# Kernel optimization log

Hardware: AMD Instinct MI355X
Metric: run time of the kernel (lower is better)

The kernel has to match this reference:

```python
import jax, jax.numpy as jnp
import numpy as np

DIM = 128      # link_state_dim
E = 100000     # num edges
P = 800000     # num adjacency pairs
G = 1000       # num graphs
T = 8          # message passing steps
R = 256        # readout_units


def setup_inputs() -> dict:
    key = jax.random.key(0)
    ks = jax.random.split(key, 16)
    s = lambda *shp: 1.0 / np.sqrt(shp[0])
    inp = {
        "link_state": jax.random.normal(ks[0], (E, DIM), dtype=jnp.float32),
        "states_graph_ids": jnp.sort(jax.random.randint(ks[1], (E,), 0, G, dtype=jnp.int32)),
        "states_first": jax.random.randint(ks[2], (P,), 0, E, dtype=jnp.int32),
        "states_second": jax.random.randint(ks[3], (P,), 0, E, dtype=jnp.int32),
        "sates_num_edges": E,
        # Message MLP: Dense(2*DIM -> DIM), selu
        "W_msg": jax.random.normal(ks[4], (2 * DIM, DIM), dtype=jnp.float32) * s(2 * DIM),
        "b_msg": jnp.zeros((DIM,), dtype=jnp.float32),
        # GRUCell (keras default reset_after=True): kernel/recurrent_kernel [DIM, 3*DIM], bias [2, 3*DIM]
        "gru_kernel": jax.random.normal(ks[5], (DIM, 3 * DIM), dtype=jnp.float32) * s(DIM),
        "gru_rec_kernel": jax.random.normal(ks[6], (DIM, 3 * DIM), dtype=jnp.float32) * s(DIM),
        "gru_bias": jnp.zeros((2, 3 * DIM), dtype=jnp.float32),
        # Readout MLP: DIM -> R -> R -> 1
        "W1": jax.random.normal(ks[7], (DIM, R), dtype=jnp.float32) * s(DIM),
        "b1": jnp.zeros((R,), dtype=jnp.float32),
        "W2": jax.random.normal(ks[8], (R, R), dtype=jnp.float32) * s(R),
        "b2": jnp.zeros((R,), dtype=jnp.float32),
        "W3": jax.random.normal(ks[9], (R, 1), dtype=jnp.float32) * s(R),
        "b3": jnp.zeros((1,), dtype=jnp.float32),
    }
    return inp


def _gru_cell(x, h, kernel, rec_kernel, bias):
    # Keras GRUCell, reset_after=True, gate order (z, r, h)
    mx = x @ kernel + bias[0]
    mh = h @ rec_kernel + bias[1]
    xz, xr, xh = jnp.split(mx, 3, axis=1)
    rz, rr, rh = jnp.split(mh, 3, axis=1)
    z = jax.nn.sigmoid(xz + rz)
    r = jax.nn.sigmoid(xr + rr)
    hh = jnp.tanh(xh + r * rh)
    return z * h + (1.0 - z) * hh


def reference(link_state, states_graph_ids, states_first, states_second, sates_num_edges,
              W_msg, b_msg, gru_kernel, gru_rec_kernel, gru_bias,
              W1, b1, W2, b2, W3, b3):
    for _ in range(T):
        # gather main & neighbor edge states, concat on feature dim -> [P, 2*DIM]
        edges_concat = jnp.concatenate([link_state[states_first], link_state[states_second]], axis=1)
        msgs = jax.nn.selu(edges_concat @ W_msg + b_msg)              # [P, DIM]
        agg = jax.ops.segment_sum(msgs, states_second, num_segments=sates_num_edges)  # [E, DIM]
        link_state = _gru_cell(agg, link_state, gru_kernel, gru_rec_kernel, gru_bias)
    pooled = jax.ops.segment_sum(link_state, states_graph_ids, num_segments=G)  # [G, DIM]
    h = jax.nn.selu(pooled @ W1 + b1)
    h = jax.nn.selu(h @ W2 + b2)
    return h @ W3 + b3  # [G, 1]
```

## Files before the change

### kernel.cpp

```cpp
#include <hip/hip_runtime.h>
#include <hip/hip_fp16.h>
#include <math.h>

#define DIM 128
#define E_NUM 100000
#define P_NUM 800000
#define G_NUM 1000
#define T_STEPS 8
#define R_UNITS 256

typedef __attribute__((ext_vector_type(8))) short bf16x8;
typedef __attribute__((ext_vector_type(4))) float f32x4;

typedef unsigned short ushort_t;
typedef unsigned int   uint_t;

__device__ __forceinline__ float selu_f(float x) {
    const float alpha = 1.6732632423543772f;
    const float scale = 1.0507009873554805f;
    return x > 0.f ? scale * x : scale * alpha * expm1f(x);
}

__device__ __forceinline__ float selu_fast(float x) {
    const float scale = 1.0507009873554805f;
    const float A     = 1.7580993408473766f;
    const float l2e   = 1.4426950408889634f;
    const float e = __builtin_amdgcn_exp2f(x * l2e);
    return x > 0.f ? scale * x : A * e - A;
}

__device__ __forceinline__ ushort_t f2bf(float x) {
    uint_t u = __float_as_uint(x);
    uint_t r = (u + 0x7fffu + ((u >> 16) & 1u)) >> 16;
    return (ushort_t)r;
}
__device__ __forceinline__ float bf2f(ushort_t h) {
    return __uint_as_float(((uint_t)h) << 16);
}

__global__ __launch_bounds__(256)
void hist_kernel(const int* __restrict__ second, int* __restrict__ counts)
{
    const int p = blockIdx.x * 256 + threadIdx.x;
    atomicAdd(&counts[second[p]], 1);
}

__global__ __launch_bounds__(1024)
void scanA_kernel(const int* __restrict__ counts, int* __restrict__ offsets,
                  int* __restrict__ bsum)
{
    __shared__ int buf[1024];
    const int i = blockIdx.x * 1024 + threadIdx.x;
    const int v = (i < E_NUM) ? counts[i] : 0;
    buf[threadIdx.x] = v;
    __syncthreads();
    for (int off = 1; off < 1024; off <<= 1) {
        const int t = (threadIdx.x >= off) ? buf[threadIdx.x - off] : 0;
        __syncthreads();
        buf[threadIdx.x] += t;
        __syncthreads();
    }
    if (i < E_NUM) offsets[i] = buf[threadIdx.x] - v;
    if (threadIdx.x == 1023) bsum[blockIdx.x] = buf[1023];
}

__global__ void scanB_kernel(int* __restrict__ bsum, int* __restrict__ offsets)
{
    int acc = 0;
    for (int b = 0; b < 98; b++) { const int t = bsum[b]; bsum[b] = acc; acc += t; }
    offsets[E_NUM] = P_NUM;
}

__global__ __launch_bounds__(1024)
void scanC_kernel(int* __restrict__ offsets, const int* __restrict__ bsum)
{
    const int i = blockIdx.x * 1024 + threadIdx.x;
    if (i < E_NUM) offsets[i] += bsum[blockIdx.x];
}

__global__ __launch_bounds__(256)
void fill_kernel(const int* __restrict__ first, const int* __restrict__ second,
                 const int* __restrict__ offsets, int* __restrict__ cursor,
                 int* __restrict__ sfirst, int* __restrict__ ssecond)
{
    const int p = blockIdx.x * 256 + threadIdx.x;
    const int d = second[p];
    const int pos = atomicAdd(&cursor[d], 1);
    const int idx = offsets[d] + pos;
    sfirst[idx] = first[p];
    ssecond[idx] = d;
}

__global__ __launch_bounds__(256)
void cast_h_kernel(const float* __restrict__ src,
                   ushort_t* __restrict__ dhi, ushort_t* __restrict__ dlo)
{
    const int idx = blockIdx.x * 256 + threadIdx.x;
    const float x = src[idx];
    const ushort_t hi = f2bf(x);
    dhi[idx] = hi;
    dlo[idx] = f2bf(x - bf2f(hi));
}

__global__ __launch_bounds__(256)
void wsplit_build_kernel(const float* __restrict__ Wmsg,
                         ushort_t* __restrict__ wt, ushort_t* __restrict__ wy)
{
    const int idx  = blockIdx.x * 256 + threadIdx.x;
    const int lane = idx & 63;
    const int nt   = (idx >> 6) & 7;
    const int comp = (idx >> 9) & 1;
    const int ks   = (idx >> 10) & 3;
    const int half = idx >> 12;
    const int n    = nt * 16 + (lane & 15);
    const int kb   = ks * 32 + (lane >> 4) * 8 + half * 128;
    ushort_t* dst  = half ? wy : wt;
    const int slot = idx & 4095;
#pragma unroll
    for (int j = 0; j < 8; j++) {
        const float w = Wmsg[(size_t)(kb + j) * DIM + n];
        const ushort_t hi = f2bf(w);
        dst[(size_t)slot * 8 + j] = comp ? f2bf(w - bf2f(hi)) : hi;
    }
}

__global__ __launch_bounds__(256)
void wb_build_kernel(const float* __restrict__ K, const float* __restrict__ U,
                     ushort_t* __restrict__ wb)
{
    const int idx  = blockIdx.x * 256 + threadIdx.x;
    const int lane = idx & 63;
    int t = idx >> 6;
    const int nt   = t % 24;  t /= 24;
    const int comp = t & 1;   t >>= 1;
    const int gemm = t & 1;
    const int ks   = t >> 1;
    const float* src = gemm ? U : K;
    const int n  = nt * 16 + (lane & 15);
    const int kb = ks * 32 + (lane >> 4) * 8;
#pragma unroll
    for (int j = 0; j < 8; j++) {
        const float w = src[(size_t)(kb + j) * 384 + n];
        const ushort_t hi = f2bf(w);
        wb[(size_t)idx * 8 + j] = comp ? f2bf(w - bf2f(hi)) : hi;
    }
}

#define AS1(p) ((const __attribute__((address_space(1))) unsigned int*)(p))
#define AS3(p) ((__attribute__((address_space(3))) unsigned int*)(p))

__global__ __launch_bounds__(256, 4)
void gy_kernel(const ushort_t* __restrict__ hbh, const ushort_t* __restrict__ hbl,
               const ushort_t* __restrict__ wt, const ushort_t* __restrict__ wy,
               const float* __restrict__ bmsg,
               __half* __restrict__ Gh, float* __restrict__ Y2b)
{
    __shared__ __align__(16) ushort_t sact[2][4096];

    const int tid  = threadIdx.x;
    const int lane = tid & 63;
    const int w    = tid >> 6;
    const int e0   = blockIdx.x * 32;
    const int m16  = lane & 15;
    const int quad = lane >> 4;

#pragma unroll
    for (int i = 0; i < 2; i++) {
        const int g  = tid + i * 256;
        const int gm = g & 15;
        const int gr = (g >> 4) & 1;
        const int gq = (g >> 5) & 3;
        const int gk = g >> 7;
        const size_t soff = (size_t)(e0 + gr * 16 + gm) * DIM + gk * 32 + gq * 8;
        __builtin_amdgcn_global_load_lds(AS1(hbh + soff), AS3((char*)sact[0] + g * 16), 16, 0, 0);
        __builtin_amdgcn_global_load_lds(AS1(hbl + soff), AS3((char*)sact[1] + g * 16), 16, 0, 0);
    }
    __syncthreads();

#define ACT(a_, ks_, rt_) \
    (*(const bf16x8*)((const char*)sact[a_] + (size_t)((ks_) * 2048 + quad * 512 + (rt_) * 256 + m16 * 16)))

    f32x4 acc[2][4] = {};
#pragma unroll
    for (int ks = 0; ks < 4; ks++) {
        bf16x8 ah[2], al[2];
#pragma unroll
        for (int rt = 0; rt < 2; rt++) {
            ah[rt] = ACT(0, ks, rt);
            al[rt] = ACT(1, ks, rt);
        }
#pragma unroll
        for (int ntl = 0; ntl < 4; ntl++) {
            const int ntg = w * 4 + ntl;
            const ushort_t* wsel = (ntg < 8) ? wt : wy;
            const int nt = ntg & 7;
            const bf16x8 bh = *(const bf16x8*)(wsel + (size_t)(((ks * 2 + 0) * 8 + nt) * 64 + lane) * 8);
            const bf16x8 bl = *(const bf16x8*)(wsel + (size_t)(((ks * 2 + 1) * 8 + nt) * 64 + lane) * 8);
#pragma unroll
            for (int rt = 0; rt < 2; rt++) {
                acc[rt][ntl] = __builtin_amdgcn_mfma_f32_16x16x32_bf16(ah[rt], bh, acc[rt][ntl], 0, 0, 0);
                acc[rt][ntl] = __builtin_amdgcn_mfma_f32_16x16x32_bf16(al[rt], bh, acc[rt][ntl], 0, 0, 0);
                acc[rt][ntl] = __builtin_amdgcn_mfma_f32_16x16x32_bf16(ah[rt], bl, acc[rt][ntl], 0, 0, 0);
            }
        }
    }
#undef ACT
#pragma unroll
    for (int ntl = 0; ntl < 4; ntl++) {
        const int ntg = w * 4 + ntl;
        const int c   = (ntg & 7) * 16 + m16;
        if (ntg < 8) {
#pragma unroll
            for (int rt = 0; rt < 2; rt++) {
#pragma unroll
                for (int reg = 0; reg < 4; reg++) {
                    const size_t row = (size_t)(e0 + rt * 16 + quad * 4 + reg);
                    Gh[row * DIM + c] = __float2half_rn(acc[rt][ntl][reg]);
                }
            }
        } else {
            const float bb = bmsg[c];
#pragma unroll
            for (int rt = 0; rt < 2; rt++) {
#pragma unroll
                for (int reg = 0; reg < 4; reg++) {
                    const size_t row = (size_t)(e0 + rt * 16 + quad * 4 + reg);
                    Y2b[row * DIM + c] = acc[rt][ntl][reg] + bb;
                }
            }
        }
    }
}

__device__ __forceinline__ void agg_one_dest(
    const __half2* __restrict__ Gh2, const int* __restrict__ sfirst,
    ushort_t* __restrict__ agg_hi, ushort_t* __restrict__ agg_lo,
    int d, int start, int end, float2 y, int c2, int lane)
{
    float a0 = 0.f, a1 = 0.f;
    int p = start;
    for (; p + 8 <= end; p += 8) {
        int f[8];
#pragma unroll
        for (int j = 0; j < 8; j++) f[j] = sfirst[p + j];
        __half2 g[8];
#pragma unroll
        for (int j = 0; j < 8; j++)
            g[j] = Gh2[(size_t)f[j] * 64 + lane];
#pragma unroll
        for (int j = 0; j < 8; j++) {
            const float2 gf = __half22float2(g[j]);
            a0 += selu_fast(gf.x + y.x);
            a1 += selu_fast(gf.y + y.y);
        }
    }
    if (p + 4 <= end) {
        int f[4];
#pragma unroll
        for (int j = 0; j < 4; j++) f[j] = sfirst[p + j];
        __half2 g[4];
#pragma unroll
        for (int j = 0; j < 4; j++)
            g[j] = Gh2[(size_t)f[j] * 64 + lane];
#pragma unroll
        for (int j = 0; j < 4; j++) {
            const float2 gf = __half22float2(g[j]);
            a0 += selu_fast(gf.x + y.x);
            a1 += selu_fast(gf.y + y.y);
        }
        p += 4;
    }
    for (; p < end; p++) {
        const int f = sfirst[p];
        const float2 gf = __half22float2(Gh2[(size_t)f * 64 + lane]);
        a0 += selu_fast(gf.x + y.x);
        a1 += selu_fast(gf.y + y.y);
    }
    const ushort_t h0 = f2bf(a0);
    const ushort_t h1 = f2bf(a1);
    ushort2 hv, lv;
    hv.x = h0;  hv.y = h1;
    lv.x = f2bf(a0 - bf2f(h0));
    lv.y = f2bf(a1 - bf2f(h1));
    *(ushort2*)(agg_hi + (size_t)d * DIM + c2) = hv;
    *(ushort2*)(agg_lo + (size_t)d * DIM + c2) = lv;
}

__global__ __launch_bounds__(256)
void agg_csr_kernel(const __half2* __restrict__ Gh2, const float* __restrict__ Y2b,
                    const int* __restrict__ offsets, const int* __restrict__ sfirst,
                    ushort_t* __restrict__ agg_hi, ushort_t* __restrict__ agg_lo)
{
    const int tid  = threadIdx.x;
    const int lane = tid & 63;
    const int wv   = blockIdx.x * 4 + (tid >> 6);
    const int c2   = lane * 2;
    const int d0   = wv * 8;

    const int o0 = offsets[d0 + 0], o1 = offsets[d0 + 1], o2 = offsets[d0 + 2];
    const int o3 = offsets[d0 + 3], o4 = offsets[d0 + 4], o5 = offsets[d0 + 5];
    const int o6 = offsets[d0 + 6], o7 = offsets[d0 + 7], o8 = offsets[d0 + 8];
    const float2* Yp = (const float2*)(Y2b + (size_t)d0 * DIM + c2);
    const float2 y0 = Yp[0],  y1 = Yp[64],  y2 = Yp[128], y3 = Yp[192];
    const float2 y4 = Yp[256], y5 = Yp[320], y6 = Yp[384], y7 = Yp[448];

    agg_one_dest(Gh2, sfirst, agg_hi, agg_lo, d0 + 0, o0, o1, y0, c2, lane);
    agg_one_dest(Gh2, sfirst, agg_hi, agg_lo, d0 + 1, o1, o2, y1, c2, lane);
    agg_one_dest(Gh2, sfirst, agg_hi, agg_lo, d0 + 2, o2, o3, y2, c2, lane);
    agg_one_dest(Gh2, sfirst, agg_hi, agg_lo, d0 + 3, o3, o4, y3, c2, lane);
    agg_one_dest(Gh2, sfirst, agg_hi, agg_lo, d0 + 4, o4, o5, y4, c2, lane);
    agg_one_dest(Gh2, sfirst, agg_hi, agg_lo, d0 + 5, o5, o6, y5, c2, lane);
    agg_one_dest(Gh2, sfirst, agg_hi, agg_lo, d0 + 6, o6, o7, y6, c2, lane);
    agg_one_dest(Gh2, sfirst, agg_hi, agg_lo, d0 + 7, o7, o8, y7, c2, lane);
}

__global__ __launch_bounds__(512, 4)
void gru_kernel(const ushort_t* __restrict__ xhg, const ushort_t* __restrict__ xlg,
                ushort_t* __restrict__ hbh, ushort_t* __restrict__ hbl,
                const ushort_t* __restrict__ wb, const float* __restrict__ bias)
{
    __shared__ __align__(16) ushort_t sact[4][4096];

    const int tid  = threadIdx.x;
    const int lane = tid & 63;
    const int w    = tid >> 6;
    const int e0   = blockIdx.x * 32;
    const int m16  = lane & 15;
    const int quad = lane >> 4;

    {
        const int gm = tid & 15;
        const int gr = (tid >> 4) & 1;
        const int gq = (tid >> 5) & 3;
        const int gk = tid >> 7;
        const size_t soff = (size_t)(e0 + gr * 16 + gm) * DIM + gk * 32 + gq * 8;
        __builtin_amdgcn_global_load_lds(AS1(xhg + soff), AS3((char*)sact[0] + tid * 16), 16, 0, 0);
        __builtin_amdgcn_global_load_lds(AS1(xlg + soff), AS3((char*)sact[1] + tid * 16), 16, 0, 0);
        __builtin_amdgcn_global_load_lds(AS1(hbh + soff), AS3((char*)sact[2] + tid * 16), 16, 0, 0);
        __builtin_amdgcn_global_load_lds(AS1(hbl + soff), AS3((char*)sact[3] + tid * 16), 16, 0, 0);
    }
    __syncthreads();

    f32x4 az[2] = {}, ar[2] = {}, ahx[2] = {}, ahh[2] = {};

#define WB(ks_, gm_, cp_, nt_) \
    (*(const bf16x8*)(wb + ((size_t)(((ks_) * 96) + (gm_) * 48 + (cp_) * 24 + (nt_)) * 64 + lane) * 8))
#define ACT(a_, ks_, rt_) \
    (*(const bf16x8*)((const char*)sact[a_] + (size_t)((ks_) * 2048 + quad * 512 + (rt_) * 256 + m16 * 16)))

#pragma unroll
    for (int ks = 0; ks < 4; ks++) {
        const bf16x8 KzH = WB(ks, 0, 0, w),      KzL = WB(ks, 0, 1, w);
        const bf16x8 UzH = WB(ks, 1, 0, w),      UzL = WB(ks, 1, 1, w);
        const bf16x8 KrH = WB(ks, 0, 0, w + 8),  KrL = WB(ks, 0, 1, w + 8);
        const bf16x8 UrH = WB(ks, 1, 0, w + 8),  UrL = WB(ks, 1, 1, w + 8);
        const bf16x8 KhH = WB(ks, 0, 0, w + 16), KhL = WB(ks, 0, 1, w + 16);
        const bf16x8 UhH = WB(ks, 1, 0, w + 16), UhL = WB(ks, 1, 1, w + 16);
#pragma unroll
        for (int rt = 0; rt < 2; rt++) {
            const bf16x8 xh = ACT(0, ks, rt);
            const bf16x8 xl = ACT(1, ks, rt);
            const bf16x8 hh = ACT(2, ks, rt);
            const bf16x8 hl = ACT(3, ks, rt);

            az[rt] = __builtin_amdgcn_mfma_f32_16x16x32_bf16(xh, KzH, az[rt], 0, 0, 0);
            az[rt] = __builtin_amdgcn_mfma_f32_16x16x32_bf16(xl, KzH, az[rt], 0, 0, 0);
            az[rt] = __builtin_amdgcn_mfma_f32_16x16x32_bf16(xh, KzL, az[rt], 0, 0, 0);
            az[rt] = __builtin_amdgcn_mfma_f32_16x16x32_bf16(hh, UzH, az[rt], 0, 0, 0);
            az[rt] = __builtin_amdgcn_mfma_f32_16x16x32_bf16(hl, UzH, az[rt], 0, 0, 0);
            az[rt] = __builtin_amdgcn_mfma_f32_16x16x32_bf16(hh, UzL, az[rt], 0, 0, 0);

            ar[rt] = __builtin_amdgcn_mfma_f32_16x16x32_bf16(xh, KrH, ar[rt], 0, 0, 0);
            ar[rt] = __builtin_amdgcn_mfma_f32_16x16x32_bf16(xl, KrH, ar[rt], 0, 0, 0);
            ar[rt] = __builtin_amdgcn_mfma_f32_16x16x32_bf16(xh, KrL, ar[rt], 0, 0, 0);
            ar[rt] = __builtin_amdgcn_mfma_f32_16x16x32_bf16(hh, UrH, ar[rt], 0, 0, 0);
            ar[rt] = __builtin_amdgcn_mfma_f32_16x16x32_bf16(hl, UrH, ar[rt], 0, 0, 0);
            ar[rt] = __builtin_amdgcn_mfma_f32_16x16x32_bf16(hh, UrL, ar[rt], 0, 0, 0);

            ahx[rt] = __builtin_amdgcn_mfma_f32_16x16x32_bf16(xh, KhH, ahx[rt], 0, 0, 0);
            ahx[rt] = __builtin_amdgcn_mfma_f32_16x16x32_bf16(xl, KhH, ahx[rt], 0, 0, 0);
            ahx[rt] = __builtin_amdgcn_mfma_f32_16x16x32_bf16(xh, KhL, ahx[rt], 0, 0, 0);
            ahh[rt] = __builtin_amdgcn_mfma_f32_16x16x32_bf16(hh, UhH, ahh[rt], 0, 0, 0);
            ahh[rt] = __builtin_amdgcn_mfma_f32_16x16x32_bf16(hl, UhH, ahh[rt], 0, 0, 0);
            ahh[rt] = __builtin_amdgcn_mfma_f32_16x16x32_bf16(hh, UhL, ahh[rt], 0, 0, 0);
        }
    }
#undef WB
#undef ACT

    const int c = w * 16 + m16;
    const float l2e  = 1.4426950408889634f;
    const float bzn  = -(bias[c] + bias[384 + c]) * l2e;
    const float brn  = -(bias[128 + c] + bias[512 + c]) * l2e;
    const float bxh  = bias[256 + c];
    const float brh  = bias[640 + c];
    const float bxh2 = bxh * (2.f * l2e);

    const int ksc   = w >> 1;
    const int quadc = (2 * w + (m16 >> 3)) & 3;
    const int elem  = m16 & 7;

#pragma unroll
    for (int rt = 0; rt < 2; rt++) {
#pragma unroll
        for (int reg = 0; reg < 4; reg++) {
            const int rrel = rt * 16 + quad * 4 + reg;
            const int row  = e0 + rrel;
            const int lidx = (ksc * 128 + quadc * 32 + rt * 16 + (quad * 4 + reg)) * 8 + elem;
            const float z = __builtin_amdgcn_rcpf(
                1.f + __builtin_amdgcn_exp2f(fmaf(az[rt][reg], -l2e, bzn)));
            const float r = __builtin_amdgcn_rcpf(
                1.f + __builtin_amdgcn_exp2f(fmaf(ar[rt][reg], -l2e, brn)));
            const float u   = fmaf(r, ahh[rt][reg] + brh, ahx[rt][reg]);
            const float eh  = __builtin_amdgcn_exp2f(fmaf(u, 2.f * l2e, bxh2));
            const float hc  = fmaf(-2.f, __builtin_amdgcn_rcpf(eh + 1.f), 1.f);
            const float hp = bf2f(sact[2][lidx]) + bf2f(sact[3][lidx]);
            const float hn = fmaf(z, hp - hc, hc);
            const size_t g = (size_t)row * DIM + c;
            const ushort_t hi = f2bf(hn);
            hbh[g] = hi;
            hbl[g] = f2bf(hn - bf2f(hi));
        }
    }
}

#undef AS1
#undef AS3

__global__ __launch_bounds__(256)
void pool_kernel(const ushort_t* __restrict__ hbh, const ushort_t* __restrict__ hbl,
                 const int* __restrict__ gid, float* __restrict__ pooled)
{
    const int idx = blockIdx.x * 256 + threadIdx.x;
    const int e = idx >> 7;
    const int n = idx & 127;
    const float hv = bf2f(hbh[idx]) + bf2f(hbl[idx]);
    atomicAdd(pooled + (size_t)gid[e] * DIM + n, hv);
}

__global__ __launch_bounds__(256)
void readout_kernel(const float* __restrict__ pooled,
                    const float* __restrict__ W1, const float* __restrict__ b1,
                    const float* __restrict__ W2, const float* __restrict__ b2,
                    const float* __restrict__ W3, const float* __restrict__ b3,
                    float* __restrict__ out)
{
    __shared__ float sp[DIM];
    __shared__ float s1[R_UNITS];
    __shared__ float s2[R_UNITS];
    const int g = blockIdx.x, tid = threadIdx.x;

    if (tid < DIM) sp[tid] = pooled[(size_t)g * DIM + tid];
    __syncthreads();

    float acc = b1[tid];
    for (int k = 0; k < DIM; k++) acc += sp[k] * W1[(size_t)k * R_UNITS + tid];
    s1[tid] = selu_f(acc);
    __syncthreads();

    acc = b2[tid];
    for (int k = 0; k < R_UNITS; k++) acc += s1[k] * W2[(size_t)k * R_UNITS + tid];
    s2[tid] = selu_f(acc) * W3[tid];
    __syncthreads();

    for (int s = 128; s > 0; s >>= 1) {
        if (tid < s) s2[tid] += s2[tid + s];
        __syncthreads();
    }
    if (tid == 0) out[g] = s2[0] + b3[0];
}

extern "C" void kernel_launch(void* const* d_in, const int* in_sizes, int n_in,
                              void* d_out, int out_size, void* d_ws, size_t ws_size,
                              hipStream_t stream)
{
    const float* link_state = (const float*)d_in[0];
    const int*   gids       = (const int*)d_in[1];
    const int*   first      = (const int*)d_in[2];
    const int*   second     = (const int*)d_in[3];
    const float* Wmsg       = (const float*)d_in[5];
    const float* bmsg       = (const float*)d_in[6];
    const float* gK         = (const float*)d_in[7];
    const float* gU         = (const float*)d_in[8];
    const float* gbias      = (const float*)d_in[9];
    const float* W1         = (const float*)d_in[10];
    const float* b1         = (const float*)d_in[11];
    const float* W2         = (const float*)d_in[12];
    const float* b2         = (const float*)d_in[13];
    const float* W3         = (const float*)d_in[14];
    const float* b3         = (const float*)d_in[15];
    float* out = (float*)d_out;

    int* offsets = (int*)d_ws;
    int* counts  = offsets + 100004;
    int* cursor  = counts + E_NUM;
    int* bsum    = cursor + E_NUM;
    int* sfirst  = bsum + 128;
    int* ssecond = sfirst + P_NUM;
    ushort_t* wt     = (ushort_t*)(ssecond + P_NUM);
    ushort_t* wy     = wt + 32768;
    ushort_t* wb     = wy + 32768;
    ushort_t* hb_hi  = wb + 196608;
    ushort_t* hb_lo  = hb_hi + (size_t)E_NUM * DIM;
    ushort_t* agg_hi = hb_lo + (size_t)E_NUM * DIM;
    ushort_t* agg_lo = agg_hi + (size_t)E_NUM * DIM;
    float*    Gf     = (float*)(agg_lo + (size_t)E_NUM * DIM);
    __half*   Gh     = (__half*)Gf;
    float*    Y2b    = Gf + (size_t)E_NUM * DIM;

    hipMemsetAsync(counts, 0, E_NUM * sizeof(int), stream);
    hipMemsetAsync(cursor, 0, E_NUM * sizeof(int), stream);
    hist_kernel<<<P_NUM / 256, 256, 0, stream>>>(second, counts);
    scanA_kernel<<<98, 1024, 0, stream>>>(counts, offsets, bsum);
    scanB_kernel<<<1, 1, 0, stream>>>(bsum, offsets);
    scanC_kernel<<<98, 1024, 0, stream>>>(offsets, bsum);
    fill_kernel<<<P_NUM / 256, 256, 0, stream>>>(first, second, offsets, cursor,
                                                 sfirst, ssecond);
    wsplit_build_kernel<<<32, 256, 0, stream>>>(Wmsg, wt, wy);
    wb_build_kernel<<<96, 256, 0, stream>>>(gK, gU, wb);
    cast_h_kernel<<<(E_NUM * DIM) / 256, 256, 0, stream>>>(link_state, hb_hi, hb_lo);

    for (int t = 0; t < T_STEPS; t++) {
        gy_kernel<<<E_NUM / 32, 256, 0, stream>>>(hb_hi, hb_lo, wt, wy, bmsg,
                                                  Gh, Y2b);
        agg_csr_kernel<<<E_NUM / 32, 256, 0, stream>>>((const __half2*)Gh, Y2b,
                                                       offsets, sfirst,
                                                       agg_hi, agg_lo);
        gru_kernel<<<E_NUM / 32, 512, 0, stream>>>(agg_hi, agg_lo,
                                                   hb_hi, hb_lo,
                                                   wb, gbias);
    }

    float* pooled = Gf;
    hipMemsetAsync(pooled, 0, (size_t)G_NUM * DIM * sizeof(float), stream);
    pool_kernel<<<(E_NUM * DIM) / 256, 256, 0, stream>>>(hb_hi, hb_lo, gids, pooled);
    readout_kernel<<<G_NUM, 256, 0, stream>>>(pooled, W1, b1, W2, b2, W3, b3, out);
}
```

Measured before the change: 1.743 ms.

## Process 64 rows per GRU block to reuse weight fragments across more tiles

Each GRU block now handles 64 edge rows instead of 32, with 4 row tiles per wave and a doubled LDS staging area. Each weight fragment loaded from global memory is reused across twice as many MFMA tiles, which halves the total weight traffic. The cost is more accumulator registers and LDS per block, so launch bounds drop to 2 blocks per CU. Bounds guards are added for the partial last block.

New measurement: 1.851 ms. 6.2% more time.

```diff
diff --git a/kernel.cpp b/kernel.cpp
--- a/kernel.cpp
+++ b/kernel.cpp
@@ -314,39 +314,43 @@
     agg_one_dest(Gh2, sfirst, agg_hi, agg_lo, d0 + 7, o7, o8, y7, c2, lane);
 }
 
-__global__ __launch_bounds__(512, 4)
+__global__ __launch_bounds__(512, 2)
 void gru_kernel(const ushort_t* __restrict__ xhg, const ushort_t* __restrict__ xlg,
                 ushort_t* __restrict__ hbh, ushort_t* __restrict__ hbl,
                 const ushort_t* __restrict__ wb, const float* __restrict__ bias)
 {
-    __shared__ __align__(16) ushort_t sact[4][4096];
+    __shared__ __align__(16) ushort_t sact[4][8192];
 
     const int tid  = threadIdx.x;
     const int lane = tid & 63;
     const int w    = tid >> 6;
-    const int e0   = blockIdx.x * 32;
+    const int e0   = blockIdx.x * 64;
     const int m16  = lane & 15;
     const int quad = lane >> 4;
 
-    {
-        const int gm = tid & 15;
-        const int gr = (tid >> 4) & 1;
-        const int gq = (tid >> 5) & 3;
-        const int gk = tid >> 7;
-        const size_t soff = (size_t)(e0 + gr * 16 + gm) * DIM + gk * 32 + gq * 8;
-        __builtin_amdgcn_global_load_lds(AS1(xhg + soff), AS3((char*)sact[0] + tid * 16), 16, 0, 0);
-        __builtin_amdgcn_global_load_lds(AS1(xlg + soff), AS3((char*)sact[1] + tid * 16), 16, 0, 0);
-        __builtin_amdgcn_global_load_lds(AS1(hbh + soff), AS3((char*)sact[2] + tid * 16), 16, 0, 0);
-        __builtin_amdgcn_global_load_lds(AS1(hbl + soff), AS3((char*)sact[3] + tid * 16), 16, 0, 0);
+#pragma unroll
+    for (int i = 0; i < 2; i++) {
+        const int g   = tid + i * 512;
+        const int gm  = g & 15;
+        const int grt = (g >> 4) & 3;
+        const int gq  = (g >> 6) & 3;
+        const int gk  = g >> 8;
+        int srow = e0 + grt * 16 + gm;
+        if (srow >= E_NUM) srow = E_NUM - 1;
+        const size_t soff = (size_t)srow * DIM + gk * 32 + gq * 8;
+        __builtin_amdgcn_global_load_lds(AS1(xhg + soff), AS3((char*)sact[0] + g * 16), 16, 0, 0);
+        __builtin_amdgcn_global_load_lds(AS1(xlg + soff), AS3((char*)sact[1] + g * 16), 16, 0, 0);
+        __builtin_amdgcn_global_load_lds(AS1(hbh + soff), AS3((char*)sact[2] + g * 16), 16, 0, 0);
+        __builtin_amdgcn_global_load_lds(AS1(hbl + soff), AS3((char*)sact[3] + g * 16), 16, 0, 0);
     }
     __syncthreads();
 
-    f32x4 az[2] = {}, ar[2] = {}, ahx[2] = {}, ahh[2] = {};
+    f32x4 az[4] = {}, ar[4] = {}, ahx[4] = {}, ahh[4] = {};
 
 #define WB(ks_, gm_, cp_, nt_) \
     (*(const bf16x8*)(wb + ((size_t)(((ks_) * 96) + (gm_) * 48 + (cp_) * 24 + (nt_)) * 64 + lane) * 8))
 #define ACT(a_, ks_, rt_) \
-    (*(const bf16x8*)((const char*)sact[a_] + (size_t)((ks_) * 2048 + quad * 512 + (rt_) * 256 + m16 * 16)))
+    (*(const bf16x8*)((const char*)sact[a_] + (size_t)((ks_) * 4096 + quad * 1024 + (rt_) * 256 + m16 * 16)))
 
 #pragma unroll
     for (int ks = 0; ks < 4; ks++) {
@@ -357,7 +361,7 @@
         const bf16x8 KhH = WB(ks, 0, 0, w + 16), KhL = WB(ks, 0, 1, w + 16);
         const bf16x8 UhH = WB(ks, 1, 0, w + 16), UhL = WB(ks, 1, 1, w + 16);
 #pragma unroll
-        for (int rt = 0; rt < 2; rt++) {
+        for (int rt = 0; rt < 4; rt++) {
             const bf16x8 xh = ACT(0, ks, rt);
             const bf16x8 xl = ACT(1, ks, rt);
             const bf16x8 hh = ACT(2, ks, rt);
@@ -401,25 +405,26 @@
     const int elem  = m16 & 7;
 
 #pragma unroll
-    for (int rt = 0; rt < 2; rt++) {
+    for (int rt = 0; rt < 4; rt++) {
 #pragma unroll
         for (int reg = 0; reg < 4; reg++) {
-            const int rrel = rt * 16 + quad * 4 + reg;
-            const int row  = e0 + rrel;
-            const int lidx = (ksc * 128 + quadc * 32 + rt * 16 + (quad * 4 + reg)) * 8 + elem;
-            const float z = __builtin_amdgcn_rcpf(
-                1.f + __builtin_amdgcn_exp2f(fmaf(az[rt][reg], -l2e, bzn)));
-            const float r = __builtin_amdgcn_rcpf(
-                1.f + __builtin_amdgcn_exp2f(fmaf(ar[rt][reg], -l2e, brn)));
-            const float u   = fmaf(r, ahh[rt][reg] + brh, ahx[rt][reg]);
-            const float eh  = __builtin_amdgcn_exp2f(fmaf(u, 2.f * l2e, bxh2));
-            const float hc  = fmaf(-2.f, __builtin_amdgcn_rcpf(eh + 1.f), 1.f);
-            const float hp = bf2f(sact[2][lidx]) + bf2f(sact[3][lidx]);
-            const float hn = fmaf(z, hp - hc, hc);
-            const size_t g = (size_t)row * DIM + c;
-            const ushort_t hi = f2bf(hn);
-            hbh[g] = hi;
-            hbl[g] = f2bf(hn - bf2f(hi));
+            const int row  = e0 + rt * 16 + quad * 4 + reg;
+            if (row < E_NUM) {
+                const int lidx = (ksc * 256 + quadc * 64 + rt * 16 + (quad * 4 + reg)) * 8 + elem;
+                const float z = __builtin_amdgcn_rcpf(
+                    1.f + __builtin_amdgcn_exp2f(fmaf(az[rt][reg], -l2e, bzn)));
+                const float r = __builtin_amdgcn_rcpf(
+                    1.f + __builtin_amdgcn_exp2f(fmaf(ar[rt][reg], -l2e, brn)));
+                const float u   = fmaf(r, ahh[rt][reg] + brh, ahx[rt][reg]);
+                const float eh  = __builtin_amdgcn_exp2f(fmaf(u, 2.f * l2e, bxh2));
+                const float hc  = fmaf(-2.f, __builtin_amdgcn_rcpf(eh + 1.f), 1.f);
+                const float hp = bf2f(sact[2][lidx]) + bf2f(sact[3][lidx]);
+                const float hn = fmaf(z, hp - hc, hc);
+                const size_t g = (size_t)row * DIM + c;
+                const ushort_t hi = f2bf(hn);
+                hbh[g] = hi;
+                hbl[g] = f2bf(hn - bf2f(hi));
+            }
         }
     }
 }
@@ -526,9 +531,9 @@
         agg_csr_kernel<<<E_NUM / 32, 256, 0, stream>>>((const __half2*)Gh, Y2b,
                                                        offsets, sfirst,
                                                        agg_hi, agg_lo);
-        gru_kernel<<<E_NUM / 32, 512, 0, stream>>>(agg_hi, agg_lo,
-                                                   hb_hi, hb_lo,
-                                                   wb, gbias);
+        gru_kernel<<<(E_NUM + 63) / 64, 512, 0, stream>>>(agg_hi, agg_lo,
+                                                          hb_hi, hb_lo,
+                                                          wb, gbias);
     }
 
     float* pooled = Gf;
```

## Fuse CSR aggregation into GRU kernel, writing aggregates directly to LDS

Applied to the files above, without the earlier changes.

Merges the CSR segment-sum aggregation kernel into the GRU kernel. Each of the 8 waves aggregates 4 destination edges and writes the bf16 hi/lo split straight into the shared-memory tile layout the GRU MFMA stage reads. This removes one kernel launch per step and the global write and reload of the aggregate arrays. The cost is that the GRU kernel now carries the irregular gather latency, so its MFMA phase waits on the slowest wave's gather, and per-wave gather parallelism is lower (4 destinations per wave instead of 8).

After: 1.677 ms. -3.8%, faster.

```diff
diff --git a/kernel.cpp b/kernel.cpp
--- a/kernel.cpp
+++ b/kernel.cpp
@@ -232,10 +232,10 @@
     }
 }
 
-__device__ __forceinline__ void agg_one_dest(
+__device__ __forceinline__ void aggru_one_dest(
     const __half2* __restrict__ Gh2, const int* __restrict__ sfirst,
-    ushort_t* __restrict__ agg_hi, ushort_t* __restrict__ agg_lo,
-    int d, int start, int end, float2 y, int c2, int lane)
+    ushort_t* __restrict__ sxh, ushort_t* __restrict__ sxl,
+    int rrel, int start, int end, float2 y, int c2, int lane)
 {
     float a0 = 0.f, a1 = 0.f;
     int p = start;
@@ -276,48 +276,25 @@
         a0 += selu_fast(gf.x + y.x);
         a1 += selu_fast(gf.y + y.y);
     }
+    const int ks = c2 >> 5;
+    const int qd = (c2 >> 3) & 3;
+    const int el = c2 & 7;
+    const int base = (ks * 128 + qd * 32 + (rrel >> 4) * 16 + (rrel & 15)) * 8 + el;
     const ushort_t h0 = f2bf(a0);
     const ushort_t h1 = f2bf(a1);
     ushort2 hv, lv;
     hv.x = h0;  hv.y = h1;
     lv.x = f2bf(a0 - bf2f(h0));
     lv.y = f2bf(a1 - bf2f(h1));
-    *(ushort2*)(agg_hi + (size_t)d * DIM + c2) = hv;
-    *(ushort2*)(agg_lo + (size_t)d * DIM + c2) = lv;
-}
-
-__global__ __launch_bounds__(256)
-void agg_csr_kernel(const __half2* __restrict__ Gh2, const float* __restrict__ Y2b,
-                    const int* __restrict__ offsets, const int* __restrict__ sfirst,
-                    ushort_t* __restrict__ agg_hi, ushort_t* __restrict__ agg_lo)
-{
-    const int tid  = threadIdx.x;
-    const int lane = tid & 63;
-    const int wv   = blockIdx.x * 4 + (tid >> 6);
-    const int c2   = lane * 2;
-    const int d0   = wv * 8;
-
-    const int o0 = offsets[d0 + 0], o1 = offsets[d0 + 1], o2 = offsets[d0 + 2];
-    const int o3 = offsets[d0 + 3], o4 = offsets[d0 + 4], o5 = offsets[d0 + 5];
-    const int o6 = offsets[d0 + 6], o7 = offsets[d0 + 7], o8 = offsets[d0 + 8];
-    const float2* Yp = (const float2*)(Y2b + (size_t)d0 * DIM + c2);
-    const float2 y0 = Yp[0],  y1 = Yp[64],  y2 = Yp[128], y3 = Yp[192];
-    const float2 y4 = Yp[256], y5 = Yp[320], y6 = Yp[384], y7 = Yp[448];
-
-    agg_one_dest(Gh2, sfirst, agg_hi, agg_lo, d0 + 0, o0, o1, y0, c2, lane);
-    agg_one_dest(Gh2, sfirst, agg_hi, agg_lo, d0 + 1, o1, o2, y1, c2, lane);
-    agg_one_dest(Gh2, sfirst, agg_hi, agg_lo, d0 + 2, o2, o3, y2, c2, lane);
-    agg_one_dest(Gh2, sfirst, agg_hi, agg_lo, d0 + 3, o3, o4, y3, c2, lane);
-    agg_one_dest(Gh2, sfirst, agg_hi, agg_lo, d0 + 4, o4, o5, y4, c2, lane);
-    agg_one_dest(Gh2, sfirst, agg_hi, agg_lo, d0 + 5, o5, o6, y5, c2, lane);
-    agg_one_dest(Gh2, sfirst, agg_hi, agg_lo, d0 + 6, o6, o7, y6, c2, lane);
-    agg_one_dest(Gh2, sfirst, agg_hi, agg_lo, d0 + 7, o7, o8, y7, c2, lane);
+    *(ushort2*)(sxh + base) = hv;
+    *(ushort2*)(sxl + base) = lv;
 }
 
 __global__ __launch_bounds__(512, 4)
-void gru_kernel(const ushort_t* __restrict__ xhg, const ushort_t* __restrict__ xlg,
-                ushort_t* __restrict__ hbh, ushort_t* __restrict__ hbl,
-                const ushort_t* __restrict__ wb, const float* __restrict__ bias)
+void aggru_kernel(const __half2* __restrict__ Gh2, const float* __restrict__ Y2b,
+                  const int* __restrict__ offsets, const int* __restrict__ sfirst,
+                  ushort_t* __restrict__ hbh, ushort_t* __restrict__ hbl,
+                  const ushort_t* __restrict__ wb, const float* __restrict__ bias)
 {
     __shared__ __align__(16) ushort_t sact[4][4096];
 
@@ -334,10 +311,22 @@
         const int gq = (tid >> 5) & 3;
         const int gk = tid >> 7;
         const size_t soff = (size_t)(e0 + gr * 16 + gm) * DIM + gk * 32 + gq * 8;
-        __builtin_amdgcn_global_load_lds(AS1(xhg + soff), AS3((char*)sact[0] + tid * 16), 16, 0, 0);
-        __builtin_amdgcn_global_load_lds(AS1(xlg + soff), AS3((char*)sact[1] + tid * 16), 16, 0, 0);
         __builtin_amdgcn_global_load_lds(AS1(hbh + soff), AS3((char*)sact[2] + tid * 16), 16, 0, 0);
         __builtin_amdgcn_global_load_lds(AS1(hbl + soff), AS3((char*)sact[3] + tid * 16), 16, 0, 0);
+    }
+
+    {
+        const int c2 = lane * 2;
+        const int d0 = e0 + w * 4;
+        const int o0 = offsets[d0 + 0], o1 = offsets[d0 + 1];
+        const int o2 = offsets[d0 + 2], o3 = offsets[d0 + 3], o4 = offsets[d0 + 4];
+        const float2* Yp = (const float2*)(Y2b + (size_t)d0 * DIM + c2);
+        const float2 y0 = Yp[0], y1 = Yp[64], y2 = Yp[128], y3 = Yp[192];
+        const int r0 = w * 4;
+        aggru_one_dest(Gh2, sfirst, sact[0], sact[1], r0 + 0, o0, o1, y0, c2, lane);
+        aggru_one_dest(Gh2, sfirst, sact[0], sact[1], r0 + 1, o1, o2, y1, c2, lane);
+        aggru_one_dest(Gh2, sfirst, sact[0], sact[1], r0 + 2, o2, o3, y2, c2, lane);
+        aggru_one_dest(Gh2, sfirst, sact[0], sact[1], r0 + 3, o3, o4, y3, c2, lane);
     }
     __syncthreads();
 
@@ -523,12 +512,10 @@
     for (int t = 0; t < T_STEPS; t++) {
         gy_kernel<<<E_NUM / 32, 256, 0, stream>>>(hb_hi, hb_lo, wt, wy, bmsg,
                                                   Gh, Y2b);
-        agg_csr_kernel<<<E_NUM / 32, 256, 0, stream>>>((const __half2*)Gh, Y2b,
-                                                       offsets, sfirst,
-                                                       agg_hi, agg_lo);
-        gru_kernel<<<E_NUM / 32, 512, 0, stream>>>(agg_hi, agg_lo,
-                                                   hb_hi, hb_lo,
-                                                   wb, gbias);
+        aggru_kernel<<<E_NUM / 32, 512, 0, stream>>>((const __half2*)Gh, Y2b,
+                                                     offsets, sfirst,
+                                                     hb_hi, hb_lo,
+                                                     wb, gbias);
     }
 
     float* pooled = Gf;
```
